# Performance work log

Measured on AMD Instinct MI355X. Metric: run time of the kernel, lower is better.

## Reference

```python
import jax, jax.numpy as jnp
import numpy as np
import math

DIM = 2048
N_HEADS = 16
HEAD_DIM = DIM // N_HEADS
B, S = 2, 2048
EPS = 1e-6


def rms_norm(x, w):
    return x * jax.lax.rsqrt(jnp.mean(x * x, axis=-1, keepdims=True) + EPS) * w


def rotate(x, cos, sin):
    x1, x2 = jnp.split(x, 2, axis=-1)
    rotated = jnp.concatenate((-x2, x1), axis=-1)
    return x * cos + rotated * sin


def setup_inputs() -> dict:
    key = jax.random.key(0)
    ks = jax.random.split(key, 16)
    half = HEAD_DIM // 2
    inv_freq = 1.0 / (10000.0 ** (jnp.arange(0, half, dtype=jnp.float32) / half))
    t = jnp.arange(S, dtype=jnp.float32)
    freqs = jnp.einsum('s,d->sd', t, inv_freq)
    emb = jnp.concatenate((freqs, freqs), axis=-1)  # [S, HEAD_DIM]
    cos = jnp.cos(emb)[None, None]  # [1,1,S,HEAD_DIM]
    sin = jnp.sin(emb)[None, None]
    # causal additive mask [1,1,S,S]
    causal = jnp.triu(jnp.full((S, S), -1e9, dtype=jnp.float32), k=1)[None, None]
    sc = 0.02
    return {
        'x': jax.random.normal(ks[0], (B, S, DIM), jnp.float32),
        'cos': cos,
        'sin': sin,
        'mask': causal,
        'attn_norm_w': jnp.ones((DIM,), jnp.float32),
        'ffn_norm_w': jnp.ones((DIM,), jnp.float32),
        'wq': jax.random.normal(ks[1], (DIM, DIM), jnp.float32) * sc,
        'wk': jax.random.normal(ks[2], (DIM, DIM), jnp.float32) * sc,
        'wv': jax.random.normal(ks[3], (DIM, DIM), jnp.float32) * sc,
        'wo': jax.random.normal(ks[4], (DIM, DIM), jnp.float32) * sc,
        'w1': jax.random.normal(ks[5], (DIM, 4 * DIM), jnp.float32) * sc,
        'w2': jax.random.normal(ks[6], (4 * DIM, DIM), jnp.float32) * sc,
        'w3': jax.random.normal(ks[7], (DIM, 4 * DIM), jnp.float32) * sc,
    }


def reference(x, cos, sin, mask, attn_norm_w, ffn_norm_w, wq, wk, wv, wo, w1, w2, w3):
    b, s, d = x.shape
    h = rms_norm(x, attn_norm_w)
    q = (h @ wq).reshape(b, s, N_HEADS, HEAD_DIM).transpose(0, 2, 1, 3)
    k = (h @ wk).reshape(b, s, N_HEADS, HEAD_DIM).transpose(0, 2, 1, 3)
    v = (h @ wv).reshape(b, s, N_HEADS, HEAD_DIM).transpose(0, 2, 1, 3)
    q = rotate(q, cos, sin)
    k = rotate(k, cos, sin)
    attn = jnp.einsum('bhqd,bhkd->bhqk', q, k) / math.sqrt(HEAD_DIM)
    attn = attn + mask
    attn = jax.nn.softmax(attn, axis=-1)
    out = jnp.einsum('bhqk,bhkd->bhqd', attn, v)
    out = out.transpose(0, 2, 1, 3).reshape(b, s, d)
    x = x + out @ wo
    h = rms_norm(x, ffn_norm_w)
    x = x + (jax.nn.silu(h @ w1) * (h @ w3)) @ w2
    return x
```

## Files before the change

### kernel.cpp

```cpp
#include <hip/hip_runtime.h>

#define DIM 2048
#define HDIM 128
#define NH 16
#define SEQ 2048
#define BATCH 2
#define MROWS (BATCH*SEQ)
#define QKP 6144

typedef __attribute__((ext_vector_type(8))) short short8;
typedef __attribute__((ext_vector_type(4))) float f32x4;

template<int N> struct ic { static constexpr int value = N; };

__device__ __forceinline__ unsigned short f2bf(float f) {
  union { float f; unsigned u; } v; v.f = f;
  unsigned r = v.u + 0x7FFFu + ((v.u >> 16) & 1u);
  return (unsigned short)(r >> 16);
}
__device__ __forceinline__ float bf2f(unsigned short b) {
  union { unsigned u; float f; } v; v.u = ((unsigned)b) << 16;
  return v.f;
}

__device__ __forceinline__ void gload16(const void* g, void* l) {
  __builtin_amdgcn_global_load_lds((const __attribute__((address_space(1))) unsigned int*)g,
                                   (__attribute__((address_space(3))) unsigned int*)l,
                                   16, 0, 0);
}

__global__ __launch_bounds__(256) void rmsnorm_kernel(const float* __restrict__ x,
                                                      const float* __restrict__ w,
                                                      unsigned short* __restrict__ out) {
  const int row = blockIdx.x;
  const int t = threadIdx.x;
  const float* xr = x + (size_t)row * DIM;
  float4 v0 = ((const float4*)xr)[t*2];
  float4 v1 = ((const float4*)xr)[t*2+1];
  float ss = v0.x*v0.x + v0.y*v0.y + v0.z*v0.z + v0.w*v0.w
           + v1.x*v1.x + v1.y*v1.y + v1.z*v1.z + v1.w*v1.w;
  #pragma unroll
  for (int i = 1; i < 64; i <<= 1) ss += __shfl_xor(ss, i);
  __shared__ float red[4];
  if ((t & 63) == 0) red[t >> 6] = ss;
  __syncthreads();
  float sum = red[0] + red[1] + red[2] + red[3];
  float sc = rsqrtf(sum * (1.0f/DIM) + 1e-6f);
  const float* wr = w + t*8;
  unsigned short ob[8];
  ob[0] = f2bf(v0.x*sc*wr[0]); ob[1] = f2bf(v0.y*sc*wr[1]);
  ob[2] = f2bf(v0.z*sc*wr[2]); ob[3] = f2bf(v0.w*sc*wr[3]);
  ob[4] = f2bf(v1.x*sc*wr[4]); ob[5] = f2bf(v1.y*sc*wr[5]);
  ob[6] = f2bf(v1.z*sc*wr[6]); ob[7] = f2bf(v1.w*sc*wr[7]);
  uint4 pk;
  pk.x = (unsigned)ob[0] | ((unsigned)ob[1] << 16);
  pk.y = (unsigned)ob[2] | ((unsigned)ob[3] << 16);
  pk.z = (unsigned)ob[4] | ((unsigned)ob[5] << 16);
  pk.w = (unsigned)ob[6] | ((unsigned)ob[7] << 16);
  *((uint4*)(out + (size_t)row*DIM + t*8)) = pk;
}

__global__ __launch_bounds__(256) void transpose_w_kernel(const float* __restrict__ W,
                                                          unsigned short* __restrict__ Wt,
                                                          int K, int N) {
  __shared__ float tile[32][33];
  const int k0 = blockIdx.x*32, n0 = blockIdx.y*32;
  const int tx = threadIdx.x, ty = threadIdx.y;
  #pragma unroll
  for (int i=0;i<4;i++) tile[ty+i*8][tx] = W[(size_t)(k0+ty+i*8)*N + n0+tx];
  __syncthreads();
  #pragma unroll
  for (int i=0;i<4;i++) Wt[(size_t)(n0+ty+i*8)*K + k0+tx] = f2bf(tile[tx][ty+i*8]);
}

__global__ __launch_bounds__(256) void transpose_v_kernel(const unsigned short* __restrict__ v,
                                                          int vpitch,
                                                          unsigned short* __restrict__ vt) {
  __shared__ unsigned short tile[32][33];
  const int b = blockIdx.z;
  const int s0 = blockIdx.x*32, c0 = blockIdx.y*32;
  const int tx = threadIdx.x, ty = threadIdx.y;
  #pragma unroll
  for (int i=0;i<4;i++) tile[ty+i*8][tx] = v[((size_t)(b*SEQ + s0+ty+i*8))*vpitch + c0+tx];
  __syncthreads();
  #pragma unroll
  for (int i=0;i<4;i++) vt[((size_t)(b*DIM + c0+ty+i*8))*SEQ + s0+tx] = tile[tx][ty+i*8];
}

__global__ __launch_bounds__(256) void rope_qk(unsigned short* __restrict__ qk,
                                               const float* __restrict__ cosb,
                                               const float* __restrict__ sinb) {
  const size_t idx = (size_t)blockIdx.x * 256 + threadIdx.x;
  const int d = (int)(idx & 63);
  const int h = (int)((idx >> 6) & 31);
  const int row = (int)(idx >> 11);
  const int s = row & (SEQ-1);
  const size_t base = (size_t)row * QKP + h*HDIM + d;
  float a  = bf2f(qk[base]);
  float bq = bf2f(qk[base+64]);
  float c1 = cosb[s*HDIM + d],    s1 = sinb[s*HDIM + d];
  float c2 = cosb[s*HDIM + d+64], s2 = sinb[s*HDIM + d+64];
  qk[base]    = f2bf(a*c1 - bq*s1);
  qk[base+64] = f2bf(bq*c2 + a*s2);
}

template<int BM, int EPI>
__global__ __launch_bounds__(512, 2) void gemm_pipe(const unsigned short* __restrict__ A,
                                                    const unsigned short* __restrict__ Bt,
                                                    const float* __restrict__ aux,
                                                    void* __restrict__ outp,
                                                    int M, int N, int K) {
  constexpr int HRA = BM/2;
  constexpr int MF  = BM/32;
  constexpr int APP = MF/4;
  constexpr int LA  = BM/128;
  constexpr int AHS = HRA*64;
  constexpr int BB  = 4*AHS;
  extern __shared__ unsigned short ldsd[];
  const int tid = threadIdx.x, l = tid & 63, wid = tid >> 6;
  const int wm = wid >> 2, wn = wid & 3;
  const int lr = l & 15, lg = l >> 4;
  const int bh = wn >> 1, brow0 = (wn & 1)*64;

  const int nbx = N >> 8;
  const int SW = (nbx >= 8) ? (nbx >> 3) : 1;
  const int xcd = (int)blockIdx.x & 7;
  const int ii  = (int)blockIdx.x >> 3;
  const int by = ii / SW;
  const int bx = xcd * SW + (ii % SW);
  const int m0 = by * BM, n0 = bx * 256;

  const int m7 = lr & 7;
  const int jks0 = ((lg    ) ^ m7) << 3;
  const int jks1 = ((4 + lg) ^ m7) << 3;
  const unsigned short* ldsA0 = ldsd + wm*AHS + lr*64;
  const unsigned short* ldsA1 = ldsA0 + 2*AHS;
  const unsigned short* ldsB0 = ldsd + BB + bh*8192 + (brow0+lr)*64;
  const unsigned short* ldsB1 = ldsB0 + 2*8192;

  const int r0 = tid >> 3;
  const int jsw = ((tid & 7) ^ (r0 & 7)) << 3;
  const unsigned short* srcA[2][LA];
  #pragma unroll
  for (int h=0;h<2;h++)
    #pragma unroll
    for (int c=0;c<LA;c++)
      srcA[h][c] = A + (size_t)(m0 + h*HRA + c*64 + r0)*K + jsw;
  const unsigned short* srcB[2][2];
  #pragma unroll
  for (int h=0;h<2;h++)
    #pragma unroll
    for (int c=0;c<2;c++)
      srcB[h][c] = Bt + (size_t)(n0 + h*128 + c*64 + r0)*K + jsw;
  unsigned short* dstL = ldsd + tid*8;

  int kO = 0;
  auto stA = [&](int db, int half, int tiled) {
    #pragma unroll
    for (int c=0;c<LA;c++)
      gload16(srcA[half][c] + kO + tiled, dstL + (db*2+half)*AHS + c*4096);
  };
  auto stB = [&](int db, int half, int tiled) {
    #pragma unroll
    for (int c=0;c<2;c++)
      gload16(srcB[half][c] + kO + tiled, dstL + BB + (db*2+half)*8192 + c*4096);
  };

  f32x4 acc[MF][4] = {};
  short8 bfrag[4][2];
  const int ntile = K >> 6;

  stB(0,0,0); stB(0,1,0);
  stA(0,0,0); stA(0,1,0);
  stB(1,0,64); stB(1,1,64);
  asm volatile("s_waitcnt vmcnt(4)" ::: "memory");
  __builtin_amdgcn_sched_barrier(0);
  __builtin_amdgcn_s_barrier();

  auto phase = [&](auto PC, auto LC) {
    constexpr int P = decltype(PC)::value;
    constexpr int LAST = decltype(LC)::value;
    constexpr int hi = P >> 2;
    constexpr int p  = P & 3;
    if constexpr (p == 0) {
      const unsigned short* bB = hi ? ldsB1 : ldsB0;
      #pragma unroll
      for (int nf=0;nf<4;nf++) {
        bfrag[nf][0] = *(const short8*)(bB + nf*1024 + jks0);
        bfrag[nf][1] = *(const short8*)(bB + nf*1024 + jks1);
      }
    }
    const unsigned short* aB = hi ? ldsA1 : ldsA0;
    short8 afr[APP][2];
    #pragma unroll
    for (int mi=0;mi<APP;mi++) {
      afr[mi][0] = *(const short8*)(aB + (p*APP+mi)*1024 + jks0);
      afr[mi][1] = *(const short8*)(aB + (p*APP+mi)*1024 + jks1);
    }
    if constexpr (P == 0)      stA(1, 0, 64);
    else if constexpr (P == 1) stA(1, 1, 64);
    else if constexpr (!LAST) {
      if constexpr (P == 2)      stB(0, 0, 128);
      else if constexpr (P == 3) stB(0, 1, 128);
      else if constexpr (P == 4) stA(0, 0, 128);
      else if constexpr (P == 5) stA(0, 1, 128);
      else if constexpr (P == 6) stB(1, 0, 192);
      else if constexpr (P == 7) stB(1, 1, 192);
    }
    if constexpr (p == 0) {
      asm volatile("s_waitcnt lgkmcnt(8)" ::: "memory");
    }
    if constexpr (P == 3) {
      if constexpr (LAST) { asm volatile("s_waitcnt vmcnt(0)" ::: "memory"); }
      else                { asm volatile("s_waitcnt vmcnt(4)" ::: "memory"); }
    }
    if constexpr (P == 7 && !LAST) {
      asm volatile("s_waitcnt vmcnt(4)" ::: "memory");
    }
    __builtin_amdgcn_s_barrier();
    asm volatile("s_waitcnt lgkmcnt(0)" ::: "memory");
    __builtin_amdgcn_sched_barrier(0);
    __builtin_amdgcn_s_setprio(1);
    #pragma unroll
    for (int mi=0;mi<APP;mi++)
      #pragma unroll
      for (int nf=0;nf<4;nf++)
        #pragma unroll
        for (int ks=0;ks<2;ks++)
          acc[p*APP+mi][nf] = __builtin_amdgcn_mfma_f32_16x16x32_bf16(afr[mi][ks], bfrag[nf][ks], acc[p*APP+mi][nf], 0,0,0);
    __builtin_amdgcn_s_setprio(0);
    __builtin_amdgcn_s_barrier();
  };

  for (int T = 0; T + 2 < ntile; T += 2, kO += 128) {
    phase(ic<0>{}, ic<0>{}); phase(ic<1>{}, ic<0>{});
    phase(ic<2>{}, ic<0>{}); phase(ic<3>{}, ic<0>{});
    phase(ic<4>{}, ic<0>{}); phase(ic<5>{}, ic<0>{});
    phase(ic<6>{}, ic<0>{}); phase(ic<7>{}, ic<0>{});
  }
  phase(ic<0>{}, ic<1>{}); phase(ic<1>{}, ic<1>{});
  phase(ic<2>{}, ic<1>{}); phase(ic<3>{}, ic<1>{});
  phase(ic<4>{}, ic<1>{}); phase(ic<5>{}, ic<1>{});
  phase(ic<6>{}, ic<1>{}); phase(ic<7>{}, ic<1>{});

  #pragma unroll
  for (int mf = 0; mf < MF; mf++)
    #pragma unroll
    for (int nf = 0; nf < 4; nf++)
      #pragma unroll
      for (int r = 0; r < 4; r++) {
        const int row = m0 + wm*HRA + mf*16 + lg*4 + r;
        const int col = n0 + wn*64 + nf*16 + lr;
        const size_t idx = (size_t)row * N + col;
        if constexpr (EPI == 0) {
          ((unsigned short*)outp)[idx] = f2bf(acc[mf][nf][r]);
        } else if constexpr (EPI == 1) {
          ((float*)outp)[idx] = acc[mf][nf][r] + aux[idx];
        } else {
          float g = acc[mf][nf][r];
          float u = bf2f(((unsigned short*)outp)[idx]);
          float sg = u / (1.0f + __expf(-u));
          ((unsigned short*)outp)[idx] = f2bf(sg * g);
        }
      }
}

__global__ __launch_bounds__(256, 2) void attn_kernel(const unsigned short* __restrict__ q,
                                                      const unsigned short* __restrict__ k,
                                                      const unsigned short* __restrict__ vt,
                                                      unsigned short* __restrict__ ao) {
  const int t = threadIdx.x, lane = t & 63, w = t >> 6;
  const int qt = (int)gridDim.x - 1 - (int)blockIdx.x;
  const int bh = blockIdx.y;
  const int b = bh >> 4, h = bh & 15;
  const int lr = lane & 15, lg = lane >> 4;
  const int q0w = qt*128 + w*32;

  __shared__ __attribute__((aligned(16))) unsigned short Kb[64*128];
  __shared__ __attribute__((aligned(16))) unsigned short Vb[128*64];
  __shared__ __attribute__((aligned(16))) unsigned short Ones[16*72];
  __shared__ __attribute__((aligned(16))) unsigned short P[4][32*72];
  unsigned short* pw = &P[w][0];

  for (int idx = t; idx < 16*72; idx += 256) Ones[idx] = (idx < 72) ? 0x3F80 : 0;

  short8 aq[2][4];
  {
    const unsigned short* qp = q + ((size_t)(b*SEQ + q0w + lr))*QKP + h*HDIM;
    #pragma unroll
    for (int mf=0;mf<2;mf++)
      #pragma unroll
      for (int c=0;c<4;c++) aq[mf][c] = *(const short8*)(qp + (size_t)mf*16*QKP + c*32 + lg*8);
  }

  f32x4 accO[2][8] = {};
  f32x4 accO9[2] = {};
  float mrow[2][4];
  #pragma unroll
  for (int mf=0;mf<2;mf++)
    #pragma unroll
    for (int r=0;r<4;r++) mrow[mf][r] = -3.0e38f;

  const float scale = 0.08838834764831845f;
  const unsigned short* kg = k + (size_t)(b*SEQ)*QKP + h*HDIM;
  const unsigned short* vg = vt + (size_t)(bh*HDIM)*SEQ;

  const unsigned short* kga[4]; const unsigned short* vga[4];
  unsigned short* kld[4]; unsigned short* vld[4];
  #pragma unroll
  for (int i=0;i<4;i++) {
    const int D = i*256 + t;
    const int rk = D >> 4, jk = D & 15;
    kga[i] = kg + (size_t)rk*QKP + ((jk ^ (rk & 7)) * 8);
    const int rv = D >> 3, jv = D & 7;
    vga[i] = vg + (size_t)rv*SEQ + ((jv ^ (rv & 7)) * 8);
    kld[i] = &Kb[i*2048 + w*512];
    vld[i] = &Vb[i*2048 + w*512];
  }

  const int KV_END = qt*128 + 128;

  for (int kv0 = 0; kv0 < KV_END; kv0 += 64) {
    #pragma unroll
    for (int i=0;i<4;i++) gload16(kga[i] + (size_t)kv0*QKP, kld[i]);
    #pragma unroll
    for (int i=0;i<4;i++) gload16(vga[i] + kv0, vld[i]);
    __syncthreads();

    if (kv0 < q0w + 32) {
      f32x4 sc[2][4] = {};
      #pragma unroll
      for (int blk=0;blk<4;blk++) {
        const int krow = blk*16 + lr;
        const int sw = (krow & 7) << 3;
        #pragma unroll
        for (int c=0;c<4;c++) {
          short8 bk = *(const short8*)&Kb[krow*128 + ((c*32 + lg*8) ^ sw)];
          sc[0][blk] = __builtin_amdgcn_mfma_f32_16x16x32_bf16(aq[0][c], bk, sc[0][blk], 0,0,0);
          sc[1][blk] = __builtin_amdgcn_mfma_f32_16x16x32_bf16(aq[1][c], bk, sc[1][blk], 0,0,0);
        }
      }
      #pragma unroll
      for (int mf=0;mf<2;mf++)
        #pragma unroll
        for (int blk=0;blk<4;blk++)
          #pragma unroll
          for (int r=0;r<4;r++) sc[mf][blk][r] *= scale;
      if (kv0 + 63 > q0w) {
        #pragma unroll
        for (int mf=0;mf<2;mf++)
          #pragma unroll
          for (int blk=0;blk<4;blk++)
            #pragma unroll
            for (int r=0;r<4;r++)
              if (kv0 + blk*16 + lr > q0w + mf*16 + lg*4 + r) sc[mf][blk][r] = -1.0e30f;
      }
      float pm[2][4];
      #pragma unroll
      for (int mf=0;mf<2;mf++)
        #pragma unroll
        for (int r=0;r<4;r++) {
          float m0 = fmaxf(fmaxf(sc[mf][0][r], sc[mf][1][r]), fmaxf(sc[mf][2][r], sc[mf][3][r]));
          #pragma unroll
          for (int x=1;x<16;x<<=1) m0 = fmaxf(m0, __shfl_xor(m0, x));
          pm[mf][r] = m0;
        }
      int need = 0;
      #pragma unroll
      for (int mf=0;mf<2;mf++)
        #pragma unroll
        for (int r=0;r<4;r++) need |= (pm[mf][r] > mrow[mf][r] + 8.0f) ? 1 : 0;
      if (__any(need)) {
        #pragma unroll
        for (int mf=0;mf<2;mf++)
          #pragma unroll
          for (int r=0;r<4;r++) {
            const float mn = fmaxf(mrow[mf][r], pm[mf][r]);
            const float fc = __expf(mrow[mf][r] - mn);
            mrow[mf][r] = mn;
            #pragma unroll
            for (int n=0;n<8;n++) accO[mf][n][r] *= fc;
            accO9[mf][r] *= fc;
          }
      }
      #pragma unroll
      for (int mf=0;mf<2;mf++)
        #pragma unroll
        for (int blk=0;blk<4;blk++)
          #pragma unroll
          for (int r=0;r<4;r++) {
            const float p = __expf(sc[mf][blk][r] - mrow[mf][r]);
            pw[(mf*16 + lg*4 + r)*72 + blk*16 + lr] = f2bf(p);
          }
      short8 ap[2][2];
      #pragma unroll
      for (int mf=0;mf<2;mf++)
        #pragma unroll
        for (int ks=0;ks<2;ks++) ap[mf][ks] = *(const short8*)&pw[(mf*16 + lr)*72 + ks*32 + lg*8];
      #pragma unroll
      for (int n=0;n<8;n++) {
        #pragma unroll
        for (int ks=0;ks<2;ks++) {
          const int vrow = n*16 + lr;
          const int sw = (vrow & 7) << 3;
          short8 bv = *(const short8*)&Vb[vrow*64 + ((ks*32 + lg*8) ^ sw)];
          accO[0][n] = __builtin_amdgcn_mfma_f32_16x16x32_bf16(ap[0][ks], bv, accO[0][n], 0,0,0);
          accO[1][n] = __builtin_amdgcn_mfma_f32_16x16x32_bf16(ap[1][ks], bv, accO[1][n], 0,0,0);
        }
      }
      #pragma unroll
      for (int ks=0;ks<2;ks++) {
        short8 bv9 = *(const short8*)&Ones[lr*72 + ks*32 + lg*8];
        accO9[0] = __builtin_amdgcn_mfma_f32_16x16x32_bf16(ap[0][ks], bv9, accO9[0], 0,0,0);
        accO9[1] = __builtin_amdgcn_mfma_f32_16x16x32_bf16(ap[1][ks], bv9, accO9[1], 0,0,0);
      }
    }
    __syncthreads();
  }

  #pragma unroll
  for (int mf=0;mf<2;mf++)
    #pragma unroll
    for (int r=0;r<4;r++) {
      const float lv = __shfl(accO9[mf][r], lane & 48);
      const float inv = 1.0f / lv;
      const size_t row = (size_t)(b*SEQ + q0w + mf*16 + lg*4 + r);
      #pragma unroll
      for (int n=0;n<8;n++)
        ao[row*DIM + h*HDIM + n*16 + lr] = f2bf(accO[mf][n][r] * inv);
    }
}

extern "C" void kernel_launch(void* const* d_in, const int* in_sizes, int n_in,
                              void* d_out, int out_size, void* d_ws, size_t ws_size,
                              hipStream_t stream) {
  (void)in_sizes; (void)n_in; (void)out_size; (void)ws_size;
  const float* x    = (const float*)d_in[0];
  const float* cosb = (const float*)d_in[1];
  const float* sinb = (const float*)d_in[2];
  const float* anw  = (const float*)d_in[4];
  const float* fnw  = (const float*)d_in[5];
  const float* wq   = (const float*)d_in[6];
  const float* wk   = (const float*)d_in[7];
  const float* wv   = (const float*)d_in[8];
  const float* wo   = (const float*)d_in[9];
  const float* w1   = (const float*)d_in[10];
  const float* w2   = (const float*)d_in[11];
  const float* w3   = (const float*)d_in[12];

  char* ws = (char*)d_ws;
  const size_t MB = 1048576;
  unsigned short* h     = (unsigned short*)(ws);
  unsigned short* qkvb  = (unsigned short*)(ws + 16*MB);
  unsigned short* mid   = qkvb;
  unsigned short* aob   = (unsigned short*)(ws + 67*MB);
  char* wt              = ws + 84*MB;
  unsigned short* wqkvT = (unsigned short*)wt;
  unsigned short* vtb   = (unsigned short*)wt;
  unsigned short* woT   = (unsigned short*)wt;
  unsigned short* wfT   = (unsigned short*)wt;
  float* x1f = (float*)d_out;

  dim3 b256(256);
  dim3 tb(32, 8);
  constexpr unsigned LDS256 = 131072;
  constexpr unsigned LDS128 = 98304;

  rmsnorm_kernel<<<dim3(MROWS), b256, 0, stream>>>(x, anw, h);

  transpose_w_kernel<<<dim3(64,64), tb, 0, stream>>>(wq, wqkvT,           2048, 2048);
  transpose_w_kernel<<<dim3(64,64), tb, 0, stream>>>(wk, wqkvT + 4194304, 2048, 2048);
  transpose_w_kernel<<<dim3(64,64), tb, 0, stream>>>(wv, wqkvT + 8388608, 2048, 2048);

  gemm_pipe<256,0><<<dim3(384), dim3(512), LDS256, stream>>>(h, wqkvT, nullptr, qkvb, MROWS, 6144, 2048);

  rope_qk<<<dim3(32768), b256, 0, stream>>>(qkvb, cosb, sinb);

  transpose_v_kernel<<<dim3(64,64,2), tb, 0, stream>>>(qkvb + 4096, QKP, vtb);

  attn_kernel<<<dim3(16,32), b256, 0, stream>>>(qkvb, qkvb + 2048, vtb, aob);

  transpose_w_kernel<<<dim3(64,64), tb, 0, stream>>>(wo, woT, 2048, 2048);
  gemm_pipe<128,1><<<dim3(256), dim3(512), LDS128, stream>>>(aob, woT, x, x1f, MROWS, 2048, 2048);

  rmsnorm_kernel<<<dim3(MROWS), b256, 0, stream>>>(x1f, fnw, h);

  transpose_w_kernel<<<dim3(64,256), tb, 0, stream>>>(w1, wfT, 2048, 8192);
  gemm_pipe<256,0><<<dim3(512), dim3(512), LDS256, stream>>>(h, wfT, nullptr, mid, MROWS, 8192, 2048);
  transpose_w_kernel<<<dim3(64,256), tb, 0, stream>>>(w3, wfT, 2048, 8192);
  gemm_pipe<256,3><<<dim3(512), dim3(512), LDS256, stream>>>(h, wfT, nullptr, mid, MROWS, 8192, 2048);

  transpose_w_kernel<<<dim3(256,64), tb, 0, stream>>>(w2, wfT, 8192, 2048);
  gemm_pipe<128,1><<<dim3(256), dim3(512), LDS128, stream>>>(mid, wfT, x1f, (float*)d_out, MROWS, 2048, 8192);
}
```

Baseline: 840.7 us.

## Restructure GEMM pipeline into two half-tile phases per k-tile

```diff
diff --git a/kernel.cpp b/kernel.cpp
--- a/kernel.cpp
+++ b/kernel.cpp
@@ -112,7 +112,7 @@
                                                     int M, int N, int K) {
   constexpr int HRA = BM/2;
   constexpr int MF  = BM/32;
-  constexpr int APP = MF/4;
+  constexpr int HMF = MF/2;
   constexpr int LA  = BM/128;
   constexpr int AHS = HRA*64;
   constexpr int BB  = 4*AHS;
@@ -155,93 +155,101 @@
   unsigned short* dstL = ldsd + tid*8;
 
   int kO = 0;
-  auto stA = [&](int db, int half, int tiled) {
-    #pragma unroll
-    for (int c=0;c<LA;c++)
-      gload16(srcA[half][c] + kO + tiled, dstL + (db*2+half)*AHS + c*4096);
+  auto stA2 = [&](int db, int tiled) {
+    #pragma unroll
+    for (int hh=0;hh<2;hh++)
+      #pragma unroll
+      for (int c=0;c<LA;c++)
+        gload16(srcA[hh][c] + kO + tiled, dstL + (db*2+hh)*AHS + c*4096);
   };
-  auto stB = [&](int db, int half, int tiled) {
-    #pragma unroll
-    for (int c=0;c<2;c++)
-      gload16(srcB[half][c] + kO + tiled, dstL + BB + (db*2+half)*8192 + c*4096);
+  auto stB2 = [&](int db, int tiled) {
+    #pragma unroll
+    for (int hh=0;hh<2;hh++)
+      #pragma unroll
+      for (int c=0;c<2;c++)
+        gload16(srcB[hh][c] + kO + tiled, dstL + BB + (db*2+hh)*8192 + c*4096);
   };
 
   f32x4 acc[MF][4] = {};
   short8 bfrag[4][2];
   const int ntile = K >> 6;
 
-  stB(0,0,0); stB(0,1,0);
-  stA(0,0,0); stA(0,1,0);
-  stB(1,0,64); stB(1,1,64);
+  stB2(0, 0);
+  stA2(0, 0);
+  stB2(1, 64);
   asm volatile("s_waitcnt vmcnt(4)" ::: "memory");
   __builtin_amdgcn_sched_barrier(0);
   __builtin_amdgcn_s_barrier();
 
-  auto phase = [&](auto PC, auto LC) {
-    constexpr int P = decltype(PC)::value;
-    constexpr int LAST = decltype(LC)::value;
-    constexpr int hi = P >> 2;
-    constexpr int p  = P & 3;
-    if constexpr (p == 0) {
-      const unsigned short* bB = hi ? ldsB1 : ldsB0;
-      #pragma unroll
-      for (int nf=0;nf<4;nf++) {
-        bfrag[nf][0] = *(const short8*)(bB + nf*1024 + jks0);
-        bfrag[nf][1] = *(const short8*)(bB + nf*1024 + jks1);
-      }
+  auto phaseA = [&](auto DC, auto MC) {
+    constexpr int D = decltype(DC)::value;
+    constexpr int MODE = decltype(MC)::value;
+    const unsigned short* bB = D ? ldsB1 : ldsB0;
+    #pragma unroll
+    for (int nf=0;nf<4;nf++) {
+      bfrag[nf][0] = *(const short8*)(bB + nf*1024 + jks0);
+      bfrag[nf][1] = *(const short8*)(bB + nf*1024 + jks1);
     }
-    const unsigned short* aB = hi ? ldsA1 : ldsA0;
-    short8 afr[APP][2];
-    #pragma unroll
-    for (int mi=0;mi<APP;mi++) {
-      afr[mi][0] = *(const short8*)(aB + (p*APP+mi)*1024 + jks0);
-      afr[mi][1] = *(const short8*)(aB + (p*APP+mi)*1024 + jks1);
+    const unsigned short* aB = D ? ldsA1 : ldsA0;
+    short8 afr[HMF][2];
+    #pragma unroll
+    for (int mi=0;mi<HMF;mi++) {
+      afr[mi][0] = *(const short8*)(aB + mi*1024 + jks0);
+      afr[mi][1] = *(const short8*)(aB + mi*1024 + jks1);
     }
-    if constexpr (P == 0)      stA(1, 0, 64);
-    else if constexpr (P == 1) stA(1, 1, 64);
-    else if constexpr (!LAST) {
-      if constexpr (P == 2)      stB(0, 0, 128);
-      else if constexpr (P == 3) stB(0, 1, 128);
-      else if constexpr (P == 4) stA(0, 0, 128);
-      else if constexpr (P == 5) stA(0, 1, 128);
-      else if constexpr (P == 6) stB(1, 0, 192);
-      else if constexpr (P == 7) stB(1, 1, 192);
-    }
-    if constexpr (p == 0) {
-      asm volatile("s_waitcnt lgkmcnt(8)" ::: "memory");
-    }
-    if constexpr (P == 3) {
-      if constexpr (LAST) { asm volatile("s_waitcnt vmcnt(0)" ::: "memory"); }
-      else                { asm volatile("s_waitcnt vmcnt(4)" ::: "memory"); }
-    }
-    if constexpr (P == 7 && !LAST) {
-      asm volatile("s_waitcnt vmcnt(4)" ::: "memory");
-    }
+    if constexpr (MODE < 2) stA2(D^1, 64 + D*64);
+    asm volatile("s_waitcnt lgkmcnt(8)" ::: "memory");
+    __builtin_amdgcn_sched_barrier(0);
     __builtin_amdgcn_s_barrier();
     asm volatile("s_waitcnt lgkmcnt(0)" ::: "memory");
     __builtin_amdgcn_sched_barrier(0);
     __builtin_amdgcn_s_setprio(1);
     #pragma unroll
-    for (int mi=0;mi<APP;mi++)
-      #pragma unroll
-      for (int nf=0;nf<4;nf++)
-        #pragma unroll
-        for (int ks=0;ks<2;ks++)
-          acc[p*APP+mi][nf] = __builtin_amdgcn_mfma_f32_16x16x32_bf16(afr[mi][ks], bfrag[nf][ks], acc[p*APP+mi][nf], 0,0,0);
+    for (int ks=0;ks<2;ks++)
+      #pragma unroll
+      for (int mi=0;mi<HMF;mi++)
+        #pragma unroll
+        for (int nf=0;nf<4;nf++)
+          acc[mi][nf] = __builtin_amdgcn_mfma_f32_16x16x32_bf16(afr[mi][ks], bfrag[nf][ks], acc[mi][nf], 0,0,0);
     __builtin_amdgcn_s_setprio(0);
     __builtin_amdgcn_s_barrier();
   };
-
-  for (int T = 0; T + 2 < ntile; T += 2, kO += 128) {
-    phase(ic<0>{}, ic<0>{}); phase(ic<1>{}, ic<0>{});
-    phase(ic<2>{}, ic<0>{}); phase(ic<3>{}, ic<0>{});
-    phase(ic<4>{}, ic<0>{}); phase(ic<5>{}, ic<0>{});
-    phase(ic<6>{}, ic<0>{}); phase(ic<7>{}, ic<0>{});
+  auto phaseB = [&](auto DC, auto MC) {
+    constexpr int D = decltype(DC)::value;
+    constexpr int MODE = decltype(MC)::value;
+    const unsigned short* aB = (D ? ldsA1 : ldsA0) + HMF*1024;
+    short8 afr[HMF][2];
+    #pragma unroll
+    for (int mi=0;mi<HMF;mi++) {
+      afr[mi][0] = *(const short8*)(aB + mi*1024 + jks0);
+      afr[mi][1] = *(const short8*)(aB + mi*1024 + jks1);
+    }
+    if constexpr (MODE == 0) stB2(D, 128 + D*64);
+    if constexpr (MODE == 0)      { asm volatile("s_waitcnt vmcnt(4)" ::: "memory"); }
+    else if constexpr (MODE == 1) { asm volatile("s_waitcnt vmcnt(0)" ::: "memory"); }
+    asm volatile("s_waitcnt lgkmcnt(4)" ::: "memory");
+    __builtin_amdgcn_sched_barrier(0);
+    __builtin_amdgcn_s_barrier();
+    asm volatile("s_waitcnt lgkmcnt(0)" ::: "memory");
+    __builtin_amdgcn_sched_barrier(0);
+    __builtin_amdgcn_s_setprio(1);
+    #pragma unroll
+    for (int ks=0;ks<2;ks++)
+      #pragma unroll
+      for (int mi=0;mi<HMF;mi++)
+        #pragma unroll
+        for (int nf=0;nf<4;nf++)
+          acc[HMF+mi][nf] = __builtin_amdgcn_mfma_f32_16x16x32_bf16(afr[mi][ks], bfrag[nf][ks], acc[HMF+mi][nf], 0,0,0);
+    __builtin_amdgcn_s_setprio(0);
+    __builtin_amdgcn_s_barrier();
+  };
+
+  for (int T = 0; T + 3 < ntile; T += 2, kO += 128) {
+    phaseA(ic<0>{}, ic<0>{}); phaseB(ic<0>{}, ic<0>{});
+    phaseA(ic<1>{}, ic<0>{}); phaseB(ic<1>{}, ic<0>{});
   }
-  phase(ic<0>{}, ic<1>{}); phase(ic<1>{}, ic<1>{});
-  phase(ic<2>{}, ic<1>{}); phase(ic<3>{}, ic<1>{});
-  phase(ic<4>{}, ic<1>{}); phase(ic<5>{}, ic<1>{});
-  phase(ic<6>{}, ic<1>{}); phase(ic<7>{}, ic<1>{});
+  phaseA(ic<0>{}, ic<1>{}); phaseB(ic<0>{}, ic<1>{});
+  phaseA(ic<1>{}, ic<2>{}); phaseB(ic<1>{}, ic<2>{});
 
   #pragma unroll
   for (int mf = 0; mf < MF; mf++)
```

After: 845.2 us. Within noise of the previous version (+0.5%).
